# Kernel optimization log

Hardware: AMD Instinct MI355X
Metric: run time of the kernel (lower is better)

Reference implementation:

```python
import jax, jax.numpy as jnp
import numpy as np

N, XC, YC, H, W_ = 1024, 512, 256, 8, 8
HID = 512


def setup_inputs() -> dict:
    key = jax.random.key(0)
    k = jax.random.split(key, 6)
    x_samples = jax.random.normal(k[0], (N, XC, H, W_), dtype=jnp.float32)
    y_samples = jax.random.normal(k[1], (N, YC, H, W_), dtype=jnp.float32)
    # p_mu: Linear(x_dim, hidden) -> ReLU -> Linear(hidden, y_dim)
    s1 = 1.0 / np.sqrt(XC)
    s2 = 1.0 / np.sqrt(HID)
    W1 = jax.random.uniform(k[2], (XC, HID), jnp.float32, -s1, s1)
    b1 = jax.random.uniform(k[3], (HID,), jnp.float32, -s1, s1)
    W2 = jax.random.uniform(k[4], (HID, YC), jnp.float32, -s2, s2)
    b2 = jax.random.uniform(k[5], (YC,), jnp.float32, -s2, s2)
    return {"x_samples": x_samples, "y_samples": y_samples,
            "W1": W1, "b1": b1, "W2": W2, "b2": b2}


def reference(x_samples, y_samples, W1, b1, W2, b2):
    # AdaptiveAvgPool2d(1) + flatten(1) == mean over spatial dims
    x_vec = x_samples.mean(axis=(2, 3))  # (N, x_dim)
    y_vec = y_samples.mean(axis=(2, 3))  # (N, y_dim)
    # p_mu MLP
    h = jax.nn.relu(x_vec @ W1 + b1)
    mu = h @ W2 + b2  # (N, y_dim)
    # positive: -(mu_i - y_i)^2 / 2, summed over D
    positive = (-((mu - y_vec) ** 2) / 2.0).sum(axis=-1)  # (N,)
    # negative: for each i, mean_j (y_j - mu_i)^2 / 2, summed over D
    diff = y_vec[None, :, :] - mu[:, None, :]  # (N, N, D)
    negative = (-(diff ** 2).mean(axis=1) / 2.0).sum(axis=-1)  # (N,)
    return (positive - negative).mean()
```

## Files before the change

### kernel.cpp

```cpp
#include <hip/hip_runtime.h>

#define N_SAMP 1024
#define XC_DIM 512
#define YC_DIM 256
#define HID_DIM 512

__global__ __launch_bounds__(256) void pool_kernel(
    const float* __restrict__ x, const float* __restrict__ y,
    float* __restrict__ x_vec, float* __restrict__ y_vec) {
  const int tid  = blockIdx.x * blockDim.x + threadIdx.x;
  const int wave = tid >> 6;
  const int lane = threadIdx.x & 63;
  const int XWAVES = (N_SAMP * XC_DIM) / 64;

  const float4* src;
  float* dst;
  long base;
  if (wave < XWAVES) {
    base = (long)wave * 64;
    src = (const float4*)x;
    dst = x_vec;
  } else {
    base = (long)(wave - XWAVES) * 64;
    src = (const float4*)y;
    dst = y_vec;
  }
  const float4* p = src + base * 16;

#pragma unroll
  for (int j = 0; j < 16; ++j) {
    float4 v = p[j * 64 + lane];
    float s = (v.x + v.y) + (v.z + v.w);
    s += __shfl_xor(s, 1);
    s += __shfl_xor(s, 2);
    s += __shfl_xor(s, 4);
    s += __shfl_xor(s, 8);
    if ((lane & 15) == 0) dst[base + j * 4 + (lane >> 4)] = s * (1.0f / 64.0f);
  }
}

#define G1_BM 64
#define G1_BN 32
#define G1_BK 16

__global__ __launch_bounds__(256) void gemm1_kernel(
    const float* __restrict__ A, const float* __restrict__ B,
    const float* __restrict__ bias, float* __restrict__ C) {
  const int K = 512, Nn = 512;
  __shared__ float As[G1_BK][G1_BM];
  __shared__ float Bs[G1_BK][G1_BN];
  const int t = threadIdx.x;
  const int bm = blockIdx.y * G1_BM;
  const int bn = blockIdx.x * G1_BN;

  const int ar = t >> 2;
  const int ac = (t & 3) * 4;
  const int br = t >> 4;
  const int bc = (t & 15) * 2;

  const int row0 = (t >> 4) * 4;
  const int col0 = (t & 15) * 2;

  float acc[4][2] = {};

  for (int k0 = 0; k0 < K; k0 += G1_BK) {
    float4 av = *(const float4*)&A[(bm + ar) * K + k0 + ac];
    float2 bv = *(const float2*)&B[(k0 + br) * Nn + bn + bc];
    __syncthreads();
    As[ac + 0][ar] = av.x;
    As[ac + 1][ar] = av.y;
    As[ac + 2][ar] = av.z;
    As[ac + 3][ar] = av.w;
    *(float2*)&Bs[br][bc] = bv;
    __syncthreads();
#pragma unroll
    for (int kk = 0; kk < G1_BK; ++kk) {
      float4 a = *(const float4*)&As[kk][row0];
      float2 b = *(const float2*)&Bs[kk][col0];
      acc[0][0] += a.x * b.x; acc[0][1] += a.x * b.y;
      acc[1][0] += a.y * b.x; acc[1][1] += a.y * b.y;
      acc[2][0] += a.z * b.x; acc[2][1] += a.z * b.y;
      acc[3][0] += a.w * b.x; acc[3][1] += a.w * b.y;
    }
  }

  const float bb0 = bias[bn + col0];
  const float bb1 = bias[bn + col0 + 1];
#pragma unroll
  for (int i = 0; i < 4; ++i) {
    float2 o;
    o.x = fmaxf(acc[i][0] + bb0, 0.0f);
    o.y = fmaxf(acc[i][1] + bb1, 0.0f);
    *(float2*)&C[(bm + row0 + i) * Nn + bn + col0] = o;
  }
}

#define G2_BM 32
#define G2_BN 32
#define G2_BK 16

__global__ __launch_bounds__(256) void gemm2_kernel(
    const float* __restrict__ A, const float* __restrict__ B,
    const float* __restrict__ bias, const float* __restrict__ yvec,
    float* __restrict__ colsum_mu, float* __restrict__ colsum_y,
    float* __restrict__ dot_out) {
  const int K = 512, Nn = 256;
  __shared__ float As[G2_BK][G2_BM];
  __shared__ float Bs[G2_BK][G2_BN];
  __shared__ float s_mu[G2_BN];
  __shared__ float s_y[G2_BN];
  const int t = threadIdx.x;
  const int bm = blockIdx.y * G2_BM;
  const int bn = blockIdx.x * G2_BN;
  if (t < G2_BN) { s_mu[t] = 0.0f; s_y[t] = 0.0f; }

  const int ar = t >> 3;
  const int ac = (t & 7) * 2;
  const int br = t >> 4;
  const int bc = (t & 15) * 2;

  const int row0 = (t >> 4) * 2;
  const int col0 = (t & 15) * 2;

  float acc[2][2] = {};

  for (int k0 = 0; k0 < K; k0 += G2_BK) {
    float2 av = *(const float2*)&A[(bm + ar) * K + k0 + ac];
    float2 bv = *(const float2*)&B[(k0 + br) * Nn + bn + bc];
    __syncthreads();
    As[ac + 0][ar] = av.x;
    As[ac + 1][ar] = av.y;
    *(float2*)&Bs[br][bc] = bv;
    __syncthreads();
#pragma unroll
    for (int kk = 0; kk < G2_BK; ++kk) {
      float2 a = *(const float2*)&As[kk][row0];
      float2 b = *(const float2*)&Bs[kk][col0];
      acc[0][0] += a.x * b.x; acc[0][1] += a.x * b.y;
      acc[1][0] += a.y * b.x; acc[1][1] += a.y * b.y;
    }
  }

  const float b2a = bias[bn + col0];
  const float b2b = bias[bn + col0 + 1];
  float dotp = 0.0f, cm0 = 0.0f, cm1 = 0.0f, cy0 = 0.0f, cy1 = 0.0f;
#pragma unroll
  for (int i = 0; i < 2; ++i) {
    const int gi = bm + row0 + i;
    float2 yv2 = *(const float2*)&yvec[gi * Nn + bn + col0];
    float mu0 = acc[i][0] + b2a;
    float mu1 = acc[i][1] + b2b;
    dotp += mu0 * yv2.x + mu1 * yv2.y;
    cm0 += mu0; cm1 += mu1;
    cy0 += yv2.x; cy1 += yv2.y;
  }
  atomicAdd(&s_mu[col0], cm0);
  atomicAdd(&s_mu[col0 + 1], cm1);
  atomicAdd(&s_y[col0], cy0);
  atomicAdd(&s_y[col0 + 1], cy1);
#pragma unroll
  for (int off = 1; off < 64; off <<= 1) dotp += __shfl_xor(dotp, off);
  if ((t & 63) == 0) atomicAdd(dot_out, dotp);
  __syncthreads();
  if (t < G2_BN) {
    atomicAdd(&colsum_mu[bn + t], s_mu[t]);
    atomicAdd(&colsum_y[bn + t], s_y[t]);
  }
}

__global__ __launch_bounds__(256) void finalize_kernel(
    const float* __restrict__ colsum_mu, const float* __restrict__ colsum_y,
    const float* __restrict__ dot_in, float* __restrict__ out) {
  __shared__ float partial[4];
  const int t = threadIdx.x;
  float v = colsum_mu[t] * colsum_y[t];
#pragma unroll
  for (int off = 1; off < 64; off <<= 1) v += __shfl_xor(v, off);
  if ((t & 63) == 0) partial[t >> 6] = v;
  __syncthreads();
  if (t == 0) {
    float tot = partial[0] + partial[1] + partial[2] + partial[3];
    out[0] = dot_in[0] * (1.0f / 1024.0f) - tot * (1.0f / (1024.0f * 1024.0f));
  }
}

extern "C" void kernel_launch(void* const* d_in, const int* in_sizes, int n_in,
                              void* d_out, int out_size, void* d_ws, size_t ws_size,
                              hipStream_t stream) {
  const float* x  = (const float*)d_in[0];
  const float* y  = (const float*)d_in[1];
  const float* W1 = (const float*)d_in[2];
  const float* b1 = (const float*)d_in[3];
  const float* W2 = (const float*)d_in[4];
  const float* b2 = (const float*)d_in[5];
  float* out = (float*)d_out;

  char* ws = (char*)d_ws;
  float* x_vec = (float*)ws;
  float* y_vec = (float*)(ws + (2u << 20));
  float* h     = (float*)(ws + (3u << 20));
  float* accum = (float*)(ws + (5u << 20));
  float* colsum_mu = accum;
  float* colsum_y  = accum + 256;
  float* dotp      = accum + 512;

  hipMemsetAsync(accum, 0, 513 * sizeof(float), stream);

  pool_kernel<<<3072, 256, 0, stream>>>(x, y, x_vec, y_vec);

  gemm1_kernel<<<dim3(16, 16), 256, 0, stream>>>(x_vec, W1, b1, h);

  gemm2_kernel<<<dim3(8, 32), 256, 0, stream>>>(h, W2, b2, y_vec,
                                                colsum_mu, colsum_y, dotp);

  finalize_kernel<<<1, 256, 0, stream>>>(colsum_mu, colsum_y, dotp, out);
}
```

Baseline: 323.9 us.

## Split-K both GEMMs with 4x4 register tiles, add reduce kernel, rework pooling

Rewrites the pooling kernel so each thread reduces one 64-element plane from 16 float4 loads, with no wave shuffles. Both GEMMs now use 64x64 tiles with 4x4 per-thread microtiles, padded shared memory, register prefetch of the next K slice, and split-K over the grid z dimension. GEMM1 writes partial sums, and GEMM2 sums those partials, adds the bias and applies ReLU while loading. A new reduce kernel sums GEMM2's partials and produces the column sums and dot product. The aim is more parallelism and higher arithmetic intensity, at the cost of extra partial-buffer traffic and one more launch.

```diff
diff --git a/kernel.cpp b/kernel.cpp
--- a/kernel.cpp
+++ b/kernel.cpp
@@ -8,164 +8,183 @@
 __global__ __launch_bounds__(256) void pool_kernel(
     const float* __restrict__ x, const float* __restrict__ y,
     float* __restrict__ x_vec, float* __restrict__ y_vec) {
-  const int tid  = blockIdx.x * blockDim.x + threadIdx.x;
-  const int wave = tid >> 6;
-  const int lane = threadIdx.x & 63;
-  const int XWAVES = (N_SAMP * XC_DIM) / 64;
-
-  const float4* src;
+  const long e = (long)blockIdx.x * 256 + threadIdx.x;
+  const long NX = (long)N_SAMP * XC_DIM;
+  const float4* p;
   float* dst;
-  long base;
-  if (wave < XWAVES) {
-    base = (long)wave * 64;
-    src = (const float4*)x;
-    dst = x_vec;
+  long o;
+  if (e < NX) {
+    p = (const float4*)x + e * 16;
+    dst = x_vec; o = e;
   } else {
-    base = (long)(wave - XWAVES) * 64;
-    src = (const float4*)y;
-    dst = y_vec;
-  }
-  const float4* p = src + base * 16;
-
-#pragma unroll
-  for (int j = 0; j < 16; ++j) {
-    float4 v = p[j * 64 + lane];
-    float s = (v.x + v.y) + (v.z + v.w);
-    s += __shfl_xor(s, 1);
-    s += __shfl_xor(s, 2);
-    s += __shfl_xor(s, 4);
-    s += __shfl_xor(s, 8);
-    if ((lane & 15) == 0) dst[base + j * 4 + (lane >> 4)] = s * (1.0f / 64.0f);
-  }
-}
-
-#define G1_BM 64
-#define G1_BN 32
-#define G1_BK 16
+    p = (const float4*)y + (e - NX) * 16;
+    dst = y_vec; o = e - NX;
+  }
+  float4 v[16];
+#pragma unroll
+  for (int j = 0; j < 16; ++j) v[j] = p[j];
+  float s0 = 0.f, s1 = 0.f, s2 = 0.f, s3 = 0.f;
+#pragma unroll
+  for (int j = 0; j < 16; j += 4) {
+    s0 += (v[j + 0].x + v[j + 0].y) + (v[j + 0].z + v[j + 0].w);
+    s1 += (v[j + 1].x + v[j + 1].y) + (v[j + 1].z + v[j + 1].w);
+    s2 += (v[j + 2].x + v[j + 2].y) + (v[j + 2].z + v[j + 2].w);
+    s3 += (v[j + 3].x + v[j + 3].y) + (v[j + 3].z + v[j + 3].w);
+  }
+  dst[o] = ((s0 + s1) + (s2 + s3)) * (1.0f / 64.0f);
+}
+
+#define TBK 16
 
 __global__ __launch_bounds__(256) void gemm1_kernel(
     const float* __restrict__ A, const float* __restrict__ B,
-    const float* __restrict__ bias, float* __restrict__ C) {
+    float* __restrict__ Hp) {
   const int K = 512, Nn = 512;
-  __shared__ float As[G1_BK][G1_BM];
-  __shared__ float Bs[G1_BK][G1_BN];
+  __shared__ float As[TBK][68];
+  __shared__ float Bs[TBK][68];
   const int t = threadIdx.x;
-  const int bm = blockIdx.y * G1_BM;
-  const int bn = blockIdx.x * G1_BN;
-
-  const int ar = t >> 2;
-  const int ac = (t & 3) * 4;
-  const int br = t >> 4;
-  const int bc = (t & 15) * 2;
-
-  const int row0 = (t >> 4) * 4;
-  const int col0 = (t & 15) * 2;
-
-  float acc[4][2] = {};
-
-  for (int k0 = 0; k0 < K; k0 += G1_BK) {
-    float4 av = *(const float4*)&A[(bm + ar) * K + k0 + ac];
-    float2 bv = *(const float2*)&B[(k0 + br) * Nn + bn + bc];
-    __syncthreads();
-    As[ac + 0][ar] = av.x;
-    As[ac + 1][ar] = av.y;
-    As[ac + 2][ar] = av.z;
-    As[ac + 3][ar] = av.w;
-    *(float2*)&Bs[br][bc] = bv;
-    __syncthreads();
-#pragma unroll
-    for (int kk = 0; kk < G1_BK; ++kk) {
+  const int bn = blockIdx.x * 64;
+  const int bm = blockIdx.y * 64;
+  const int ks = blockIdx.z;
+
+  const int arow = t >> 2, acol = (t & 3) * 4;
+  const int brow = t >> 4, bcol = (t & 15) * 4;
+  const int row0 = (t >> 4) * 4, col0 = (t & 15) * 4;
+
+  float acc[4][4] = {};
+  const int k0 = ks * 128;
+
+  float4 av = *(const float4*)&A[(bm + arow) * K + k0 + acol];
+  float4 bv = *(const float4*)&B[(k0 + brow) * Nn + bn + bcol];
+
+  for (int it = 0; it < 8; ++it) {
+    __syncthreads();
+    As[acol + 0][arow] = av.x;
+    As[acol + 1][arow] = av.y;
+    As[acol + 2][arow] = av.z;
+    As[acol + 3][arow] = av.w;
+    *(float4*)&Bs[brow][bcol] = bv;
+    __syncthreads();
+    if (it < 7) {
+      const int k1 = k0 + (it + 1) * TBK;
+      av = *(const float4*)&A[(bm + arow) * K + k1 + acol];
+      bv = *(const float4*)&B[(k1 + brow) * Nn + bn + bcol];
+    }
+#pragma unroll
+    for (int kk = 0; kk < TBK; ++kk) {
       float4 a = *(const float4*)&As[kk][row0];
-      float2 b = *(const float2*)&Bs[kk][col0];
-      acc[0][0] += a.x * b.x; acc[0][1] += a.x * b.y;
-      acc[1][0] += a.y * b.x; acc[1][1] += a.y * b.y;
-      acc[2][0] += a.z * b.x; acc[2][1] += a.z * b.y;
-      acc[3][0] += a.w * b.x; acc[3][1] += a.w * b.y;
-    }
-  }
-
-  const float bb0 = bias[bn + col0];
-  const float bb1 = bias[bn + col0 + 1];
+      float4 b = *(const float4*)&Bs[kk][col0];
+      acc[0][0] += a.x * b.x; acc[0][1] += a.x * b.y; acc[0][2] += a.x * b.z; acc[0][3] += a.x * b.w;
+      acc[1][0] += a.y * b.x; acc[1][1] += a.y * b.y; acc[1][2] += a.y * b.z; acc[1][3] += a.y * b.w;
+      acc[2][0] += a.z * b.x; acc[2][1] += a.z * b.y; acc[2][2] += a.z * b.z; acc[2][3] += a.z * b.w;
+      acc[3][0] += a.w * b.x; acc[3][1] += a.w * b.y; acc[3][2] += a.w * b.z; acc[3][3] += a.w * b.w;
+    }
+  }
+
+  float* H = Hp + (long)ks * (N_SAMP * HID_DIM);
 #pragma unroll
   for (int i = 0; i < 4; ++i) {
-    float2 o;
-    o.x = fmaxf(acc[i][0] + bb0, 0.0f);
-    o.y = fmaxf(acc[i][1] + bb1, 0.0f);
-    *(float2*)&C[(bm + row0 + i) * Nn + bn + col0] = o;
-  }
-}
-
-#define G2_BM 32
-#define G2_BN 32
-#define G2_BK 16
+    float4 o;
+    o.x = acc[i][0]; o.y = acc[i][1]; o.z = acc[i][2]; o.w = acc[i][3];
+    *(float4*)&H[(long)(bm + row0 + i) * Nn + bn + col0] = o;
+  }
+}
 
 __global__ __launch_bounds__(256) void gemm2_kernel(
-    const float* __restrict__ A, const float* __restrict__ B,
-    const float* __restrict__ bias, const float* __restrict__ yvec,
-    float* __restrict__ colsum_mu, float* __restrict__ colsum_y,
-    float* __restrict__ dot_out) {
+    const float* __restrict__ Hp, const float* __restrict__ b1,
+    const float* __restrict__ B, float* __restrict__ Mup) {
   const int K = 512, Nn = 256;
-  __shared__ float As[G2_BK][G2_BM];
-  __shared__ float Bs[G2_BK][G2_BN];
-  __shared__ float s_mu[G2_BN];
-  __shared__ float s_y[G2_BN];
+  __shared__ float As[TBK][68];
+  __shared__ float Bs[TBK][68];
   const int t = threadIdx.x;
-  const int bm = blockIdx.y * G2_BM;
-  const int bn = blockIdx.x * G2_BN;
-  if (t < G2_BN) { s_mu[t] = 0.0f; s_y[t] = 0.0f; }
-
-  const int ar = t >> 3;
-  const int ac = (t & 7) * 2;
-  const int br = t >> 4;
-  const int bc = (t & 15) * 2;
-
-  const int row0 = (t >> 4) * 2;
-  const int col0 = (t & 15) * 2;
-
-  float acc[2][2] = {};
-
-  for (int k0 = 0; k0 < K; k0 += G2_BK) {
-    float2 av = *(const float2*)&A[(bm + ar) * K + k0 + ac];
-    float2 bv = *(const float2*)&B[(k0 + br) * Nn + bn + bc];
-    __syncthreads();
-    As[ac + 0][ar] = av.x;
-    As[ac + 1][ar] = av.y;
-    *(float2*)&Bs[br][bc] = bv;
-    __syncthreads();
-#pragma unroll
-    for (int kk = 0; kk < G2_BK; ++kk) {
-      float2 a = *(const float2*)&As[kk][row0];
-      float2 b = *(const float2*)&Bs[kk][col0];
-      acc[0][0] += a.x * b.x; acc[0][1] += a.x * b.y;
-      acc[1][0] += a.y * b.x; acc[1][1] += a.y * b.y;
-    }
-  }
-
-  const float b2a = bias[bn + col0];
-  const float b2b = bias[bn + col0 + 1];
-  float dotp = 0.0f, cm0 = 0.0f, cm1 = 0.0f, cy0 = 0.0f, cy1 = 0.0f;
-#pragma unroll
-  for (int i = 0; i < 2; ++i) {
-    const int gi = bm + row0 + i;
-    float2 yv2 = *(const float2*)&yvec[gi * Nn + bn + col0];
-    float mu0 = acc[i][0] + b2a;
-    float mu1 = acc[i][1] + b2b;
-    dotp += mu0 * yv2.x + mu1 * yv2.y;
-    cm0 += mu0; cm1 += mu1;
-    cy0 += yv2.x; cy1 += yv2.y;
-  }
-  atomicAdd(&s_mu[col0], cm0);
-  atomicAdd(&s_mu[col0 + 1], cm1);
-  atomicAdd(&s_y[col0], cy0);
-  atomicAdd(&s_y[col0 + 1], cy1);
-#pragma unroll
-  for (int off = 1; off < 64; off <<= 1) dotp += __shfl_xor(dotp, off);
-  if ((t & 63) == 0) atomicAdd(dot_out, dotp);
-  __syncthreads();
-  if (t < G2_BN) {
-    atomicAdd(&colsum_mu[bn + t], s_mu[t]);
-    atomicAdd(&colsum_y[bn + t], s_y[t]);
-  }
+  const int bn = blockIdx.x * 64;
+  const int bm = blockIdx.y * 64;
+  const int ks = blockIdx.z;
+
+  const int arow = t >> 2, acol = (t & 3) * 4;
+  const int brow = t >> 4, bcol = (t & 15) * 4;
+  const int row0 = (t >> 4) * 4, col0 = (t & 15) * 4;
+  const long HS = (long)N_SAMP * HID_DIM;
+
+  float acc[4][4] = {};
+  const int k0 = ks * 64;
+
+  long aidx = (long)(bm + arow) * K + k0 + acol;
+  float4 a0 = *(const float4*)&Hp[aidx];
+  float4 a1 = *(const float4*)&Hp[aidx + HS];
+  float4 a2 = *(const float4*)&Hp[aidx + 2 * HS];
+  float4 a3 = *(const float4*)&Hp[aidx + 3 * HS];
+  float4 bb = *(const float4*)&b1[k0 + acol];
+  float4 bv = *(const float4*)&B[(k0 + brow) * Nn + bn + bcol];
+
+  for (int it = 0; it < 4; ++it) {
+    float4 av;
+    av.x = fmaxf(a0.x + a1.x + a2.x + a3.x + bb.x, 0.0f);
+    av.y = fmaxf(a0.y + a1.y + a2.y + a3.y + bb.y, 0.0f);
+    av.z = fmaxf(a0.z + a1.z + a2.z + a3.z + bb.z, 0.0f);
+    av.w = fmaxf(a0.w + a1.w + a2.w + a3.w + bb.w, 0.0f);
+    __syncthreads();
+    As[acol + 0][arow] = av.x;
+    As[acol + 1][arow] = av.y;
+    As[acol + 2][arow] = av.z;
+    As[acol + 3][arow] = av.w;
+    *(float4*)&Bs[brow][bcol] = bv;
+    __syncthreads();
+    if (it < 3) {
+      const int k1 = k0 + (it + 1) * TBK;
+      aidx = (long)(bm + arow) * K + k1 + acol;
+      a0 = *(const float4*)&Hp[aidx];
+      a1 = *(const float4*)&Hp[aidx + HS];
+      a2 = *(const float4*)&Hp[aidx + 2 * HS];
+      a3 = *(const float4*)&Hp[aidx + 3 * HS];
+      bb = *(const float4*)&b1[k1 + acol];
+      bv = *(const float4*)&B[(k1 + brow) * Nn + bn + bcol];
+    }
+#pragma unroll
+    for (int kk = 0; kk < TBK; ++kk) {
+      float4 a = *(const float4*)&As[kk][row0];
+      float4 b = *(const float4*)&Bs[kk][col0];
+      acc[0][0] += a.x * b.x; acc[0][1] += a.x * b.y; acc[0][2] += a.x * b.z; acc[0][3] += a.x * b.w;
+      acc[1][0] += a.y * b.x; acc[1][1] += a.y * b.y; acc[1][2] += a.y * b.z; acc[1][3] += a.y * b.w;
+      acc[2][0] += a.z * b.x; acc[2][1] += a.z * b.y; acc[2][2] += a.z * b.z; acc[2][3] += a.z * b.w;
+      acc[3][0] += a.w * b.x; acc[3][1] += a.w * b.y; acc[3][2] += a.w * b.z; acc[3][3] += a.w * b.w;
+    }
+  }
+
+  float* M = Mup + (long)ks * (N_SAMP * YC_DIM);
+#pragma unroll
+  for (int i = 0; i < 4; ++i) {
+    float4 o;
+    o.x = acc[i][0]; o.y = acc[i][1]; o.z = acc[i][2]; o.w = acc[i][3];
+    *(float4*)&M[(long)(bm + row0 + i) * Nn + bn + col0] = o;
+  }
+}
+
+__global__ __launch_bounds__(256) void reduce_kernel(
+    const float* __restrict__ Mup, const float* __restrict__ b2,
+    const float* __restrict__ yv, float* __restrict__ colsum_mu,
+    float* __restrict__ colsum_y, float* __restrict__ dot_out) {
+  const int d = threadIdx.x;
+  const int n0 = blockIdx.x * 4;
+  const long MS = (long)N_SAMP * YC_DIM;
+  const float bb = b2[d];
+  float cm = 0.f, cy = 0.f, dp = 0.f;
+#pragma unroll
+  for (int r = 0; r < 4; ++r) {
+    const long idx = (long)(n0 + r) * YC_DIM + d;
+    float mu = bb;
+#pragma unroll
+    for (int s = 0; s < 8; ++s) mu += Mup[idx + s * MS];
+    const float yy = yv[idx];
+    dp += mu * yy;
+    cm += mu;
+    cy += yy;
+  }
+  atomicAdd(&colsum_mu[d], cm);
+  atomicAdd(&colsum_y[d], cy);
+#pragma unroll
+  for (int off = 1; off < 64; off <<= 1) dp += __shfl_xor(dp, off);
+  if ((d & 63) == 0) atomicAdd(dot_out, dp);
 }
 
 __global__ __launch_bounds__(256) void finalize_kernel(
@@ -197,9 +216,10 @@
 
   char* ws = (char*)d_ws;
   float* x_vec = (float*)ws;
-  float* y_vec = (float*)(ws + (2u << 20));
-  float* h     = (float*)(ws + (3u << 20));
-  float* accum = (float*)(ws + (5u << 20));
+  float* y_vec = (float*)(ws + (2lu << 20));
+  float* Hp    = (float*)(ws + (4lu << 20));
+  float* Mup   = (float*)(ws + (12lu << 20));
+  float* accum = (float*)(ws + (20lu << 20));
   float* colsum_mu = accum;
   float* colsum_y  = accum + 256;
   float* dotp      = accum + 512;
@@ -208,10 +228,12 @@
 
   pool_kernel<<<3072, 256, 0, stream>>>(x, y, x_vec, y_vec);
 
-  gemm1_kernel<<<dim3(16, 16), 256, 0, stream>>>(x_vec, W1, b1, h);
-
-  gemm2_kernel<<<dim3(8, 32), 256, 0, stream>>>(h, W2, b2, y_vec,
-                                                colsum_mu, colsum_y, dotp);
+  gemm1_kernel<<<dim3(8, 16, 4), 256, 0, stream>>>(x_vec, W1, Hp);
+
+  gemm2_kernel<<<dim3(4, 16, 8), 256, 0, stream>>>(Hp, b1, W2, Mup);
+
+  reduce_kernel<<<256, 256, 0, stream>>>(Mup, b2, y_vec, colsum_mu,
+                                         colsum_y, dotp);
 
   finalize_kernel<<<1, 256, 0, stream>>>(colsum_mu, colsum_y, dotp, out);
 }
```

After: 282.0 us. 12.9% less time.
